# Optimization experiments

Measured on AMD Instinct MI355X. Metric: run time of the kernel, lower is better.

## Reference

```python
import jax, jax.numpy as jnp
import numpy as np

EPS = 1e-12  # torch F.normalize clamp_min eps


def _linear_interp(t, M):
    # PyTorch F.interpolate(mode='linear', align_corners=False) along last axis.
    L = t.shape[-1]
    src = (jnp.arange(M, dtype=t.dtype) + 0.5) * (L / M) - 0.5
    src = jnp.maximum(src, 0.0)
    i0 = jnp.minimum(jnp.floor(src).astype(jnp.int32), L - 1)
    i1 = jnp.minimum(i0 + 1, L - 1)
    frac = src - i0.astype(t.dtype)
    return t[..., i0] * (1.0 - frac) + t[..., i1] * frac


def _l2norm(t):
    n = jnp.linalg.norm(t, axis=-1, keepdims=True)
    return t / jnp.maximum(n, EPS)


def setup_inputs() -> dict:
    key = jax.random.key(0)
    ks = jax.random.split(key, 6)
    b, dim, m = 4, 512, 4096
    h = w = 64
    heads = 8
    s = 0.02
    return {
        "x": jax.random.normal(ks[0], (b, dim, m), dtype=jnp.float32),
        "y": jax.random.normal(ks[1], (b, dim, h, w), dtype=jnp.float32),
        "temperature": jnp.ones((heads, 1, 1), dtype=jnp.float32),
        "w_kv": jax.random.normal(ks[2], (2 * dim, dim), dtype=jnp.float32) * s,
        "w_q": jax.random.normal(ks[3], (dim, dim), dtype=jnp.float32) * s,
        "w_dw": jax.random.normal(ks[4], (dim, dim, 3, 3), dtype=jnp.float32) * s,
        "w_out": jax.random.normal(ks[5], (dim, dim), dtype=jnp.float32) * s,
    }


def reference(x, y, temperature, w_kv, w_q, w_dw, w_out):
    b, c, m = x.shape
    heads = temperature.shape[0]
    hd = c // heads

    # kv = Conv1d(dim, 2*dim, k=1)(x); split into k, v
    kv = jnp.einsum('bcm,oc->bom', x, w_kv)
    k, v = jnp.split(kv, 2, axis=1)

    # q = dwconv3x3(Conv2d 1x1(y)) -> flatten -> linear-resize to m
    q = jnp.einsum('bchw,oc->bohw', y, w_q)
    q = jax.lax.conv_general_dilated(
        q, w_dw, window_strides=(1, 1), padding=[(1, 1), (1, 1)],
        dimension_numbers=('NCHW', 'OIHW', 'NCHW'))
    q = q.reshape(b, c, -1)
    q = _linear_interp(q, m)

    # split heads: [b, head, c', m]
    q = _l2norm(q.reshape(b, heads, hd, m))
    k = _l2norm(k.reshape(b, heads, hd, m))
    v = v.reshape(b, heads, hd, m)

    # channel-wise attention: [b, head, c', c']
    attn = jnp.einsum('bhcm,bhdm->bhcd', q, k) * temperature
    attn = jax.nn.softmax(attn, axis=-1)
    out = jnp.einsum('bhcd,bhdm->bhcm', attn, v).reshape(b, c, m)

    # project_out: Conv1d k=1
    return jnp.einsum('bcm,oc->bom', out, w_out)
```

## Files before the change

### kernel.cpp

```cpp
#include <hip/hip_runtime.h>
#include <hip/hip_bf16.h>
#include <math.h>

typedef float f32x4 __attribute__((ext_vector_type(4)));
typedef int   i32x4 __attribute__((ext_vector_type(4)));
typedef short s16x8 __attribute__((ext_vector_type(8)));

#define NB 4
#define NC 512
#define NM 4096
#define NHEADS 8

#define GLDS16(src, dst) __builtin_amdgcn_global_load_lds( \
    (const __attribute__((address_space(1))) void*)(src),  \
    (__attribute__((address_space(3))) void*)(dst), 16, 0, 0)

__device__ __forceinline__ float b2f(unsigned short u) {
  union { unsigned int i; float f; } x; x.i = ((unsigned)u) << 16; return x.f;
}

__global__ __launch_bounds__(256) void transpose_k(
    const float* __restrict__ x, const float* __restrict__ y,
    __hip_bfloat16* __restrict__ xT, __hip_bfloat16* __restrict__ yT)
{
  __shared__ __hip_bfloat16 tile[64][65];
  int z = blockIdx.z;
  const float* src = ((z < 4) ? x : y) + (long)(z & 3) * ((long)NC * NM);
  __hip_bfloat16* dst = (z < 4 ? xT : yT) + (long)(z & 3) * ((long)NC * NM);
  int tm = blockIdx.x * 64, tc = blockIdx.y * 64;
  int tx = threadIdx.x & 63, ty = threadIdx.x >> 6;
  #pragma unroll
  for (int p = 0; p < 16; p++) {
    int row = ty + p * 4;
    tile[row][tx] = __float2bfloat16(src[(long)(tc + row) * NM + tm + tx]);
  }
  __syncthreads();
  #pragma unroll
  for (int p = 0; p < 16; p++) {
    int row = ty + p * 4;
    dst[(long)(tm + row) * NC + tc + tx] = tile[tx][row];
  }
}

__global__ __launch_bounds__(256) void pack_wdw(
    const float* __restrict__ wdw, __hip_bfloat16* __restrict__ Wr)
{
  long idx = (long)blockIdx.x * 256 + threadIdx.x;
  if (idx < 9L * 512 * 512) {
    int r = (int)(idx >> 18);
    int rem = (int)(idx & 262143);
    int o = rem >> 9, i = rem & 511;
    Wr[idx] = __float2bfloat16(wdw[((long)o * 512 + i) * 9 + r]);
  }
}

__global__ __launch_bounds__(256) void convert_w(
    const float* __restrict__ wkv, const float* __restrict__ wq,
    __hip_bfloat16* __restrict__ wkvB, __hip_bfloat16* __restrict__ wqT)
{
  long idx = (long)blockIdx.x * 256 + threadIdx.x;
  if (idx < 524288) {
    wkvB[idx] = __float2bfloat16(wkv[idx]);
  } else if (idx < 524288 + 262144) {
    long j = idx - 524288;
    int c = (int)(j >> 9), cp = (int)(j & 511);
    wqT[j] = __float2bfloat16(wq[(long)cp * 512 + c]);
  }
}

__global__ __launch_bounds__(256) void gemm_bt(
    const __hip_bfloat16* __restrict__ Aall, long sA,
    const __hip_bfloat16* __restrict__ Ball, long sB,
    __hip_bfloat16* __restrict__ Cball, float* __restrict__ Cfall, long sC,
    int M, int N, int Kd, int outF32)
{
  const __hip_bfloat16* A = Aall + (long)blockIdx.z * sA;
  const __hip_bfloat16* B = Ball + (long)blockIdx.z * sB;
  const int m0 = blockIdx.y * 128, n0 = blockIdx.x * 128;
  __shared__ __hip_bfloat16 As[128 * 32];
  __shared__ __hip_bfloat16 Bs[128 * 32];
  const int tid = threadIdx.x;
  const int wid = tid >> 6, lane = tid & 63;
  const int wm = (wid >> 1) * 64, wn = (wid & 1) * 64;
  const int quad = lane >> 4, l16 = lane & 15;
  const int srow = wid * 32 + (lane >> 2);
  const int scol = (lane & 3) * 8;
  f32x4 acc[4][4] = {};
  for (int k0 = 0; k0 < Kd; k0 += 32) {
    __syncthreads();
    #pragma unroll
    for (int t = 0; t < 2; t++) {
      GLDS16(A + (long)(m0 + srow + t * 16) * Kd + k0 + scol,
             As + (wid * 32 + t * 16) * 32);
      GLDS16(B + (long)(n0 + srow + t * 16) * Kd + k0 + scol,
             Bs + (wid * 32 + t * 16) * 32);
    }
    __builtin_amdgcn_s_waitcnt(0);
    __syncthreads();
    s16x8 bfr[4];
    #pragma unroll
    for (int j = 0; j < 4; j++)
      bfr[j] = *(const s16x8*)(&Bs[(wn + j * 16 + l16) * 32 + quad * 8]);
    #pragma unroll
    for (int i = 0; i < 4; i++) {
      s16x8 af = *(const s16x8*)(&As[(wm + i * 16 + l16) * 32 + quad * 8]);
      #pragma unroll
      for (int j = 0; j < 4; j++)
        acc[i][j] = __builtin_amdgcn_mfma_f32_16x16x32_bf16(af, bfr[j], acc[i][j], 0, 0, 0);
    }
  }
  if (outF32) {
    float* C = Cfall + (long)blockIdx.z * sC;
    #pragma unroll
    for (int i = 0; i < 4; i++)
      #pragma unroll
      for (int j = 0; j < 4; j++) {
        int rbase = m0 + wm + i * 16 + quad * 4;
        int col = n0 + wn + j * 16 + l16;
        #pragma unroll
        for (int r = 0; r < 4; r++)
          C[(long)(rbase + r) * N + col] = acc[i][j][r];
      }
  } else {
    __hip_bfloat16* C = Cball + (long)blockIdx.z * sC;
    #pragma unroll
    for (int i = 0; i < 4; i++)
      #pragma unroll
      for (int j = 0; j < 4; j++) {
        int rbase = m0 + wm + i * 16 + quad * 4;
        int col = n0 + wn + j * 16 + l16;
        #pragma unroll
        for (int r = 0; r < 4; r++)
          C[(long)(rbase + r) * N + col] = __float2bfloat16(acc[i][j][r]);
      }
  }
}

__global__ __launch_bounds__(256) void conv3x3(
    const __hip_bfloat16* __restrict__ Wt,
    const __hip_bfloat16* __restrict__ yT,
    const __hip_bfloat16* __restrict__ zeropad,
    __hip_bfloat16* __restrict__ q2)
{
  const int b = blockIdx.z;
  const int n0 = blockIdx.x * 128;
  const int m0 = blockIdx.y * 128;
  __shared__ __hip_bfloat16 As3[3 * 128 * 32];
  __shared__ __hip_bfloat16 Bs[256 * 32];
  const int tid = threadIdx.x;
  const int wid = tid >> 6, lane = tid & 63;
  const int wm = (wid >> 1) * 64, wn = (wid & 1) * 64;
  const int quad = lane >> 4, l16 = lane & 15;
  const int lrow = lane >> 2, scol = (lane & 3) * 8;
  const int h0 = n0 >> 6;
  const __hip_bfloat16* yb = yT + (long)b * NM * NC;
  f32x4 acc[4][4] = {};
  const s16x8 zero8 = {0, 0, 0, 0, 0, 0, 0, 0};

  for (int ic = 0; ic < 512; ic += 32) {
    #pragma unroll
    for (int g = 0; g < 3; g++) {
      __syncthreads();
      if (g == 0) {
        #pragma unroll
        for (int t = 0; t < 4; t++) {
          int p = wid * 64 + t * 16 + lrow;
          int hw = (h0 - 1) * 64 + p;
          const __hip_bfloat16* src = (((unsigned)hw) < (unsigned)NM)
              ? (yb + (long)hw * NC + ic + scol) : (zeropad + scol % 8);
          GLDS16(src, Bs + (wid * 64 + t * 16) * 32);
        }
      }
      #pragma unroll
      for (int t = 0; t < 3; t++) {
        int r = g * 3 + t;
        #pragma unroll
        for (int t2 = 0; t2 < 2; t2++) {
          GLDS16(Wt + ((long)r * 512 + m0 + wid * 32 + t2 * 16 + lrow) * 512 + ic + scol,
                 As3 + (t * 128 + wid * 32 + t2 * 16) * 32);
        }
      }
      __builtin_amdgcn_s_waitcnt(0);
      __syncthreads();
      const int dy = g - 1;
      #pragma unroll
      for (int t = 0; t < 3; t++) {
        const int dx = t - 1;
        s16x8 bfr[4];
        #pragma unroll
        for (int j = 0; j < 4; j++) {
          int nl = wn + j * 16 + l16;
          int wq_ = nl & 63, hr = nl >> 6;
          int wp = wq_ + dx;
          bool v = ((unsigned)wp) < 64u;
          int p = v ? ((hr + 1 + dy) * 64 + wp) : 0;
          s16x8 tt = *(const s16x8*)(&Bs[p * 32 + quad * 8]);
          bfr[j] = v ? tt : zero8;
        }
        #pragma unroll
        for (int i = 0; i < 4; i++) {
          s16x8 af = *(const s16x8*)(&As3[(t * 128 + wm + i * 16 + l16) * 32 + quad * 8]);
          #pragma unroll
          for (int j = 0; j < 4; j++)
            acc[i][j] = __builtin_amdgcn_mfma_f32_16x16x32_bf16(af, bfr[j], acc[i][j], 0, 0, 0);
        }
      }
    }
  }
  __hip_bfloat16* Cb = q2 + (long)b * NC * NM;
  #pragma unroll
  for (int i = 0; i < 4; i++) {
    #pragma unroll
    for (int j = 0; j < 4; j++) {
      int rbase = m0 + wm + i * 16 + quad * 4;
      int col = n0 + wn + j * 16 + l16;
      #pragma unroll
      for (int r = 0; r < 4; r++)
        Cb[(long)(rbase + r) * NM + col] = __float2bfloat16(acc[i][j][r]);
    }
  }
}

__global__ __launch_bounds__(256) void rowsumsq(
    const __hip_bfloat16* __restrict__ X, float* __restrict__ out)
{
  long row = blockIdx.x;
  const __hip_bfloat16* p = X + row * (long)NM + threadIdx.x * 16;
  union { i32x4 v; unsigned short u[8]; } a, b;
  a.v = *(const i32x4*)(p);
  b.v = *(const i32x4*)(p + 8);
  float s = 0.f;
  #pragma unroll
  for (int t = 0; t < 8; t++) {
    float f0 = b2f(a.u[t]); s += f0 * f0;
    float f1 = b2f(b.u[t]); s += f1 * f1;
  }
  #pragma unroll
  for (int off = 32; off > 0; off >>= 1) s += __shfl_down(s, off);
  __shared__ float red[4];
  if ((threadIdx.x & 63) == 0) red[threadIdx.x >> 6] = s;
  __syncthreads();
  if (threadIdx.x == 0)
    out[row] = fmaxf(sqrtf(red[0] + red[1] + red[2] + red[3]), 1e-12f);
}

__global__ __launch_bounds__(256) void attn_g(
    const __hip_bfloat16* __restrict__ q2, const __hip_bfloat16* __restrict__ Kb,
    float* __restrict__ Gpart)
{
  const int mc = blockIdx.x, h = blockIdx.y, b = blockIdx.z;
  const __hip_bfloat16* qrow = q2 + ((long)b * NC + h * 64) * NM + mc * 512;
  const __hip_bfloat16* krow = Kb + ((long)b * NC + h * 64) * NM + mc * 512;
  __shared__ __hip_bfloat16 Qs[64 * 40];
  __shared__ __hip_bfloat16 Ks[64 * 40];
  const int tid = threadIdx.x;
  const int wid = tid >> 6, lane = tid & 63;
  const int wc = (wid >> 1) * 32, wd = (wid & 1) * 32;
  const int quad = lane >> 4, l16 = lane & 15;
  const int srow = tid >> 2, scol = (tid & 3) * 8;
  f32x4 acc[2][2] = {};
  for (int k0 = 0; k0 < 512; k0 += 32) {
    __syncthreads();
    *(i32x4*)(&Qs[srow * 40 + scol]) = *(const i32x4*)(&qrow[(long)srow * NM + k0 + scol]);
    *(i32x4*)(&Ks[srow * 40 + scol]) = *(const i32x4*)(&krow[(long)srow * NM + k0 + scol]);
    __syncthreads();
    s16x8 bfr[2];
    #pragma unroll
    for (int j = 0; j < 2; j++)
      bfr[j] = *(const s16x8*)(&Ks[(wd + j * 16 + l16) * 40 + quad * 8]);
    #pragma unroll
    for (int i = 0; i < 2; i++) {
      s16x8 af = *(const s16x8*)(&Qs[(wc + i * 16 + l16) * 40 + quad * 8]);
      #pragma unroll
      for (int j = 0; j < 2; j++)
        acc[i][j] = __builtin_amdgcn_mfma_f32_16x16x32_bf16(af, bfr[j], acc[i][j], 0, 0, 0);
    }
  }
  float* gp = Gpart + ((long)((b * 8 + h) * 8 + mc)) * 4096;
  #pragma unroll
  for (int i = 0; i < 2; i++)
    #pragma unroll
    for (int j = 0; j < 2; j++)
      #pragma unroll
      for (int r = 0; r < 4; r++)
        gp[(wc + i * 16 + quad * 4 + r) * 64 + wd + j * 16 + l16] = acc[i][j][r];
}

__global__ __launch_bounds__(256) void softmax_attn(
    const float* __restrict__ Gpart, const float* __restrict__ qn,
    const float* __restrict__ kn, const float* __restrict__ temp,
    float* __restrict__ attn)
{
  const int h = blockIdx.x, b = blockIdx.y;
  __shared__ float G[64][64];
  const int tid = threadIdx.x;
  const float tv = temp[h];
  for (int e = tid; e < 4096; e += 256) {
    float s = 0.f;
    #pragma unroll
    for (int p = 0; p < 8; p++)
      s += Gpart[((long)((b * 8 + h) * 8 + p)) * 4096 + e];
    int c = e >> 6, d = e & 63;
    float scale = tv / (qn[b * 512 + h * 64 + c] * kn[b * 512 + h * 64 + d]);
    G[c][d] = s * scale;
  }
  __syncthreads();
  int row = tid >> 2, s4 = tid & 3;
  float mx = -1e30f;
  for (int d = s4; d < 64; d += 4) mx = fmaxf(mx, G[row][d]);
  mx = fmaxf(mx, __shfl_xor(mx, 1));
  mx = fmaxf(mx, __shfl_xor(mx, 2));
  float sum = 0.f;
  for (int d = s4; d < 64; d += 4) { float e = __expf(G[row][d] - mx); G[row][d] = e; sum += e; }
  sum += __shfl_xor(sum, 1);
  sum += __shfl_xor(sum, 2);
  float inv = 1.f / sum;
  float* ap = attn + ((long)(b * 8 + h)) * 4096;
  for (int d = s4; d < 64; d += 4) ap[row * 64 + d] = G[row][d] * inv;
}

__global__ __launch_bounds__(256) void wa_kernel(
    const float* __restrict__ attn, const float* __restrict__ wout,
    __hip_bfloat16* __restrict__ Wa)
{
  const int oc = blockIdx.x, h = blockIdx.y, b = blockIdx.z;
  __shared__ float At[64][64];
  __shared__ float Wtl[64][65];
  const int tid = threadIdx.x;
  const float* ap = attn + ((long)(b * 8 + h)) * 4096;
  for (int e = tid; e < 4096; e += 256) {
    At[e >> 6][e & 63] = ap[e];
    Wtl[e >> 6][e & 63] = wout[(long)(oc * 64 + (e >> 6)) * 512 + h * 64 + (e & 63)];
  }
  __syncthreads();
  int d = tid & 63, og = tid >> 6;
  #pragma unroll
  for (int k = 0; k < 16; k++) {
    int o = og * 16 + k;
    float s = 0.f;
    #pragma unroll 8
    for (int c = 0; c < 64; c++) s += Wtl[o][c] * At[c][d];
    Wa[((long)b * 512 + oc * 64 + o) * 512 + h * 64 + d] = __float2bfloat16(s);
  }
}

extern "C" void kernel_launch(void* const* d_in, const int* in_sizes, int n_in,
                              void* d_out, int out_size, void* d_ws, size_t ws_size,
                              hipStream_t stream) {
  const float* x    = (const float*)d_in[0];
  const float* y    = (const float*)d_in[1];
  const float* temp = (const float*)d_in[2];
  const float* wkv  = (const float*)d_in[3];
  const float* wq   = (const float*)d_in[4];
  const float* wdw  = (const float*)d_in[5];
  const float* wout = (const float*)d_in[6];
  float* out = (float*)d_out;

  char* ws = (char*)d_ws;
  const long TEN = 16777216;
  __hip_bfloat16* xT  = (__hip_bfloat16*)(ws);
  __hip_bfloat16* q2  = xT;
  __hip_bfloat16* yT  = (__hip_bfloat16*)(ws + TEN);
  float* Gpart        = (float*)(ws + TEN);
  float* attn         = (float*)(ws + TEN + 4194304);
  __hip_bfloat16* Wa  = (__hip_bfloat16*)(ws + TEN + 4718592);
  float* knorm        = (float*)(ws + TEN + 6815744);
  float* qnorm        = (float*)(ws + TEN + 6823936);
  __hip_bfloat16* Kb  = (__hip_bfloat16*)(ws + 2 * TEN);
  __hip_bfloat16* Vt  = (__hip_bfloat16*)(ws + 3 * TEN);
  __hip_bfloat16* Wfold = (__hip_bfloat16*)(ws + 4 * TEN);
  __hip_bfloat16* Wr    = (__hip_bfloat16*)(ws + 4 * TEN + 4718592);
  __hip_bfloat16* wkvB  = (__hip_bfloat16*)(ws + 4 * TEN + 9437184);
  __hip_bfloat16* wqT   = (__hip_bfloat16*)(ws + 4 * TEN + 10485760);
  __hip_bfloat16* zeropad = (__hip_bfloat16*)(ws + 4 * TEN + 11010048);

  const long S = (long)4096 * 512;
  const long S2 = (long)512 * 512;
  dim3 blk(256);

  hipMemsetAsync(zeropad, 0, 256, stream);
  pack_wdw<<<dim3(9216), blk, 0, stream>>>(wdw, Wr);
  convert_w<<<dim3(3072), blk, 0, stream>>>(wkv, wq, wkvB, wqT);
  transpose_k<<<dim3(64, 8, 8), blk, 0, stream>>>(x, y, xT, yT);
  gemm_bt<<<dim3(4, 4, 9), blk, 0, stream>>>(Wr, S2, wqT, 0L, Wfold, nullptr, S2, 512, 512, 512, 0);
  gemm_bt<<<dim3(32, 4, 4), blk, 0, stream>>>(wkvB, 0L, xT, S, Kb, nullptr, S, 512, 4096, 512, 0);
  gemm_bt<<<dim3(4, 32, 4), blk, 0, stream>>>(xT, S, wkvB + 512 * 512, 0L, Vt, nullptr, S, 4096, 512, 512, 0);
  conv3x3<<<dim3(32, 4, 4), blk, 0, stream>>>(Wfold, yT, zeropad, q2);
  rowsumsq<<<dim3(2048), blk, 0, stream>>>(Kb, knorm);
  rowsumsq<<<dim3(2048), blk, 0, stream>>>(q2, qnorm);
  attn_g<<<dim3(8, 8, 4), blk, 0, stream>>>(q2, Kb, Gpart);
  softmax_attn<<<dim3(8, 4), blk, 0, stream>>>(Gpart, qnorm, knorm, temp, attn);
  wa_kernel<<<dim3(8, 8, 4), blk, 0, stream>>>(attn, wout, Wa);
  gemm_bt<<<dim3(32, 4, 4), blk, 0, stream>>>(Wa, S2, Vt, S, nullptr, out, S, 512, 4096, 512, 1);
  (void)in_sizes; (void)n_in; (void)out_size; (void)ws_size;
}
```

Measured before the change: 321.5 us.

## Fuse norms into GEMM epilogues, merge prep kernels, K/V GEMM, and softmax with Wa

Row sum-of-squares for K and Q are now accumulated with atomics in the GEMM and conv epilogues, which removes two separate rowsumsq passes over bf16 tensors. The weight-conversion kernels and the memset are merged into one prep kernel that also zeroes the norm buffers. K and V projections run in one gemm_kv launch, and softmax is fused with the Wa computation. The transpose is vectorized with float4 loads and ushort4 stores. In exchange, the norms now come from fp32 accumulators rather than rounded bf16 values, the atomics make summation order nondeterministic, and the softmax is recomputed redundantly in each of the eight oc blocks.

```diff
diff --git a/kernel.cpp b/kernel.cpp
--- a/kernel.cpp
+++ b/kernel.cpp
@@ -15,56 +15,59 @@
     (const __attribute__((address_space(1))) void*)(src),  \
     (__attribute__((address_space(3))) void*)(dst), 16, 0, 0)
 
-__device__ __forceinline__ float b2f(unsigned short u) {
-  union { unsigned int i; float f; } x; x.i = ((unsigned)u) << 16; return x.f;
+__global__ __launch_bounds__(256) void prep(
+    const float* __restrict__ wdw, const float* __restrict__ wkv,
+    const float* __restrict__ wq,
+    __hip_bfloat16* __restrict__ Wr, __hip_bfloat16* __restrict__ wkvB,
+    __hip_bfloat16* __restrict__ wqT, __hip_bfloat16* __restrict__ zeropad,
+    float* __restrict__ norms)
+{
+  long idx = (long)blockIdx.x * 256 + threadIdx.x;
+  if (idx < 2359296) {
+    int r = (int)(idx / 262144);
+    int rem = (int)(idx % 262144);
+    int o = rem >> 9, i = rem & 511;
+    Wr[idx] = __float2bfloat16(wdw[((long)o * 512 + i) * 9 + r]);
+  } else if (idx < 2883584) {
+    long j = idx - 2359296;
+    wkvB[j] = __float2bfloat16(wkv[j]);
+  } else if (idx < 3145728) {
+    long j = idx - 2883584;
+    int c = (int)(j >> 9), cp = (int)(j & 511);
+    wqT[j] = __float2bfloat16(wq[(long)cp * 512 + c]);
+  } else if (idx < 3145856) {
+    zeropad[idx - 3145728] = __float2bfloat16(0.f);
+  } else if (idx < 3149952) {
+    norms[idx - 3145856] = 0.f;
+  }
 }
 
 __global__ __launch_bounds__(256) void transpose_k(
     const float* __restrict__ x, const float* __restrict__ y,
     __hip_bfloat16* __restrict__ xT, __hip_bfloat16* __restrict__ yT)
 {
-  __shared__ __hip_bfloat16 tile[64][65];
+  __shared__ __hip_bfloat16 tile[64][68];
   int z = blockIdx.z;
   const float* src = ((z < 4) ? x : y) + (long)(z & 3) * ((long)NC * NM);
   __hip_bfloat16* dst = (z < 4 ? xT : yT) + (long)(z & 3) * ((long)NC * NM);
   int tm = blockIdx.x * 64, tc = blockIdx.y * 64;
-  int tx = threadIdx.x & 63, ty = threadIdx.x >> 6;
-  #pragma unroll
-  for (int p = 0; p < 16; p++) {
-    int row = ty + p * 4;
-    tile[row][tx] = __float2bfloat16(src[(long)(tc + row) * NM + tm + tx]);
+  int tx4 = threadIdx.x & 15, trow = threadIdx.x >> 4;
+  #pragma unroll
+  for (int p = 0; p < 4; p++) {
+    int crow = trow + p * 16;
+    f32x4 v = *(const f32x4*)&src[(long)(tc + crow) * NM + tm + tx4 * 4];
+    #pragma unroll
+    for (int t = 0; t < 4; t++) tile[crow][tx4 * 4 + t] = __float2bfloat16(v[t]);
   }
   __syncthreads();
   #pragma unroll
-  for (int p = 0; p < 16; p++) {
-    int row = ty + p * 4;
-    dst[(long)(tm + row) * NC + tc + tx] = tile[tx][row];
-  }
-}
-
-__global__ __launch_bounds__(256) void pack_wdw(
-    const float* __restrict__ wdw, __hip_bfloat16* __restrict__ Wr)
-{
-  long idx = (long)blockIdx.x * 256 + threadIdx.x;
-  if (idx < 9L * 512 * 512) {
-    int r = (int)(idx >> 18);
-    int rem = (int)(idx & 262143);
-    int o = rem >> 9, i = rem & 511;
-    Wr[idx] = __float2bfloat16(wdw[((long)o * 512 + i) * 9 + r]);
-  }
-}
-
-__global__ __launch_bounds__(256) void convert_w(
-    const float* __restrict__ wkv, const float* __restrict__ wq,
-    __hip_bfloat16* __restrict__ wkvB, __hip_bfloat16* __restrict__ wqT)
-{
-  long idx = (long)blockIdx.x * 256 + threadIdx.x;
-  if (idx < 524288) {
-    wkvB[idx] = __float2bfloat16(wkv[idx]);
-  } else if (idx < 524288 + 262144) {
-    long j = idx - 524288;
-    int c = (int)(j >> 9), cp = (int)(j & 511);
-    wqT[j] = __float2bfloat16(wq[(long)cp * 512 + c]);
+  for (int p = 0; p < 4; p++) {
+    int mrow = trow + p * 16;
+    union { ushort4 u4; unsigned short u[4]; } o;
+    #pragma unroll
+    for (int t = 0; t < 4; t++)
+      o.u[t] = *(const unsigned short*)&tile[tx4 * 4 + t][mrow];
+    *(ushort4*)&dst[(long)(tm + mrow) * NC + tc + tx4 * 4] = o.u4;
   }
 }
 
@@ -136,11 +139,88 @@
   }
 }
 
+__global__ __launch_bounds__(256) void gemm_kv(
+    const __hip_bfloat16* __restrict__ wkvB,
+    const __hip_bfloat16* __restrict__ xT,
+    __hip_bfloat16* __restrict__ Kb,
+    __hip_bfloat16* __restrict__ Vt,
+    float* __restrict__ knorm2)
+{
+  const int z = blockIdx.z;
+  const int b = z & 3;
+  const bool kmode = (z < 4);
+  const long S = (long)NM * NC;
+  const __hip_bfloat16* A = kmode ? wkvB : (xT + b * S);
+  const __hip_bfloat16* B = kmode ? (xT + b * S) : (wkvB + 262144);
+  __hip_bfloat16* C = kmode ? (Kb + b * S) : (Vt + b * S);
+  const int m0 = (kmode ? blockIdx.y : blockIdx.x) * 128;
+  const int n0 = (kmode ? blockIdx.x : blockIdx.y) * 128;
+  const int N = kmode ? NM : NC;
+  __shared__ __hip_bfloat16 As[128 * 32];
+  __shared__ __hip_bfloat16 Bs[128 * 32];
+  const int tid = threadIdx.x;
+  const int wid = tid >> 6, lane = tid & 63;
+  const int wm = (wid >> 1) * 64, wn = (wid & 1) * 64;
+  const int quad = lane >> 4, l16 = lane & 15;
+  const int srow = wid * 32 + (lane >> 2);
+  const int scol = (lane & 3) * 8;
+  f32x4 acc[4][4] = {};
+  for (int k0 = 0; k0 < NC; k0 += 32) {
+    __syncthreads();
+    #pragma unroll
+    for (int t = 0; t < 2; t++) {
+      GLDS16(A + (long)(m0 + srow + t * 16) * NC + k0 + scol,
+             As + (wid * 32 + t * 16) * 32);
+      GLDS16(B + (long)(n0 + srow + t * 16) * NC + k0 + scol,
+             Bs + (wid * 32 + t * 16) * 32);
+    }
+    __builtin_amdgcn_s_waitcnt(0);
+    __syncthreads();
+    s16x8 bfr[4];
+    #pragma unroll
+    for (int j = 0; j < 4; j++)
+      bfr[j] = *(const s16x8*)(&Bs[(wn + j * 16 + l16) * 32 + quad * 8]);
+    #pragma unroll
+    for (int i = 0; i < 4; i++) {
+      s16x8 af = *(const s16x8*)(&As[(wm + i * 16 + l16) * 32 + quad * 8]);
+      #pragma unroll
+      for (int j = 0; j < 4; j++)
+        acc[i][j] = __builtin_amdgcn_mfma_f32_16x16x32_bf16(af, bfr[j], acc[i][j], 0, 0, 0);
+    }
+  }
+  #pragma unroll
+  for (int i = 0; i < 4; i++)
+    #pragma unroll
+    for (int j = 0; j < 4; j++) {
+      int rbase = m0 + wm + i * 16 + quad * 4;
+      int col = n0 + wn + j * 16 + l16;
+      #pragma unroll
+      for (int r = 0; r < 4; r++)
+        C[(long)(rbase + r) * N + col] = __float2bfloat16(acc[i][j][r]);
+    }
+  if (kmode) {
+    #pragma unroll
+    for (int i = 0; i < 4; i++) {
+      int rbase = m0 + wm + i * 16 + quad * 4;
+      #pragma unroll
+      for (int r = 0; r < 4; r++) {
+        float s = 0.f;
+        #pragma unroll
+        for (int j = 0; j < 4; j++) s += acc[i][j][r] * acc[i][j][r];
+        s += __shfl_xor(s, 1); s += __shfl_xor(s, 2);
+        s += __shfl_xor(s, 4); s += __shfl_xor(s, 8);
+        if (l16 == 0) atomicAdd(&knorm2[b * 512 + rbase + r], s);
+      }
+    }
+  }
+}
+
 __global__ __launch_bounds__(256) void conv3x3(
     const __hip_bfloat16* __restrict__ Wt,
     const __hip_bfloat16* __restrict__ yT,
     const __hip_bfloat16* __restrict__ zeropad,
-    __hip_bfloat16* __restrict__ q2)
+    __hip_bfloat16* __restrict__ q2,
+    float* __restrict__ qnorm2)
 {
   const int b = blockIdx.z;
   const int n0 = blockIdx.x * 128;
@@ -209,7 +289,7 @@
   }
   __hip_bfloat16* Cb = q2 + (long)b * NC * NM;
   #pragma unroll
-  for (int i = 0; i < 4; i++) {
+  for (int i = 0; i < 4; i++)
     #pragma unroll
     for (int j = 0; j < 4; j++) {
       int rbase = m0 + wm + i * 16 + quad * 4;
@@ -218,30 +298,19 @@
       for (int r = 0; r < 4; r++)
         Cb[(long)(rbase + r) * NM + col] = __float2bfloat16(acc[i][j][r]);
     }
-  }
-}
-
-__global__ __launch_bounds__(256) void rowsumsq(
-    const __hip_bfloat16* __restrict__ X, float* __restrict__ out)
-{
-  long row = blockIdx.x;
-  const __hip_bfloat16* p = X + row * (long)NM + threadIdx.x * 16;
-  union { i32x4 v; unsigned short u[8]; } a, b;
-  a.v = *(const i32x4*)(p);
-  b.v = *(const i32x4*)(p + 8);
-  float s = 0.f;
-  #pragma unroll
-  for (int t = 0; t < 8; t++) {
-    float f0 = b2f(a.u[t]); s += f0 * f0;
-    float f1 = b2f(b.u[t]); s += f1 * f1;
-  }
-  #pragma unroll
-  for (int off = 32; off > 0; off >>= 1) s += __shfl_down(s, off);
-  __shared__ float red[4];
-  if ((threadIdx.x & 63) == 0) red[threadIdx.x >> 6] = s;
-  __syncthreads();
-  if (threadIdx.x == 0)
-    out[row] = fmaxf(sqrtf(red[0] + red[1] + red[2] + red[3]), 1e-12f);
+  #pragma unroll
+  for (int i = 0; i < 4; i++) {
+    int rbase = m0 + wm + i * 16 + quad * 4;
+    #pragma unroll
+    for (int r = 0; r < 4; r++) {
+      float s = 0.f;
+      #pragma unroll
+      for (int j = 0; j < 4; j++) s += acc[i][j][r] * acc[i][j][r];
+      s += __shfl_xor(s, 1); s += __shfl_xor(s, 2);
+      s += __shfl_xor(s, 4); s += __shfl_xor(s, 8);
+      if (l16 == 0) atomicAdd(&qnorm2[b * 512 + rbase + r], s);
+    }
+  }
 }
 
 __global__ __launch_bounds__(256) void attn_g(
@@ -286,13 +355,14 @@
         gp[(wc + i * 16 + quad * 4 + r) * 64 + wd + j * 16 + l16] = acc[i][j][r];
 }
 
-__global__ __launch_bounds__(256) void softmax_attn(
-    const float* __restrict__ Gpart, const float* __restrict__ qn,
-    const float* __restrict__ kn, const float* __restrict__ temp,
-    float* __restrict__ attn)
-{
-  const int h = blockIdx.x, b = blockIdx.y;
+__global__ __launch_bounds__(256) void softmax_wa(
+    const float* __restrict__ Gpart, const float* __restrict__ qnorm2,
+    const float* __restrict__ knorm2, const float* __restrict__ temp,
+    const float* __restrict__ wout, __hip_bfloat16* __restrict__ Wa)
+{
+  const int oc = blockIdx.x, h = blockIdx.y, b = blockIdx.z;
   __shared__ float G[64][64];
+  __shared__ float Wt[64][65];
   const int tid = threadIdx.x;
   const float tv = temp[h];
   for (int e = tid; e < 4096; e += 256) {
@@ -301,8 +371,10 @@
     for (int p = 0; p < 8; p++)
       s += Gpart[((long)((b * 8 + h) * 8 + p)) * 4096 + e];
     int c = e >> 6, d = e & 63;
-    float scale = tv / (qn[b * 512 + h * 64 + c] * kn[b * 512 + h * 64 + d]);
-    G[c][d] = s * scale;
+    float qn = fmaxf(sqrtf(qnorm2[b * 512 + h * 64 + c]), 1e-12f);
+    float kn = fmaxf(sqrtf(knorm2[b * 512 + h * 64 + d]), 1e-12f);
+    G[c][d] = s * tv / (qn * kn);
+    Wt[c][d] = wout[(long)(oc * 64 + c) * 512 + h * 64 + d];
   }
   __syncthreads();
   int row = tid >> 2, s4 = tid & 3;
@@ -315,31 +387,15 @@
   sum += __shfl_xor(sum, 1);
   sum += __shfl_xor(sum, 2);
   float inv = 1.f / sum;
-  float* ap = attn + ((long)(b * 8 + h)) * 4096;
-  for (int d = s4; d < 64; d += 4) ap[row * 64 + d] = G[row][d] * inv;
-}
-
-__global__ __launch_bounds__(256) void wa_kernel(
-    const float* __restrict__ attn, const float* __restrict__ wout,
-    __hip_bfloat16* __restrict__ Wa)
-{
-  const int oc = blockIdx.x, h = blockIdx.y, b = blockIdx.z;
-  __shared__ float At[64][64];
-  __shared__ float Wtl[64][65];
-  const int tid = threadIdx.x;
-  const float* ap = attn + ((long)(b * 8 + h)) * 4096;
-  for (int e = tid; e < 4096; e += 256) {
-    At[e >> 6][e & 63] = ap[e];
-    Wtl[e >> 6][e & 63] = wout[(long)(oc * 64 + (e >> 6)) * 512 + h * 64 + (e & 63)];
-  }
+  for (int d = s4; d < 64; d += 4) G[row][d] *= inv;
   __syncthreads();
   int d = tid & 63, og = tid >> 6;
   #pragma unroll
-  for (int k = 0; k < 16; k++) {
-    int o = og * 16 + k;
+  for (int k2 = 0; k2 < 16; k2++) {
+    int o = og * 16 + k2;
     float s = 0.f;
     #pragma unroll 8
-    for (int c = 0; c < 64; c++) s += Wtl[o][c] * At[c][d];
+    for (int c = 0; c < 64; c++) s += Wt[o][c] * G[c][d];
     Wa[((long)b * 512 + oc * 64 + o) * 512 + h * 64 + d] = __float2bfloat16(s);
   }
 }
@@ -362,10 +418,7 @@
   __hip_bfloat16* q2  = xT;
   __hip_bfloat16* yT  = (__hip_bfloat16*)(ws + TEN);
   float* Gpart        = (float*)(ws + TEN);
-  float* attn         = (float*)(ws + TEN + 4194304);
   __hip_bfloat16* Wa  = (__hip_bfloat16*)(ws + TEN + 4718592);
-  float* knorm        = (float*)(ws + TEN + 6815744);
-  float* qnorm        = (float*)(ws + TEN + 6823936);
   __hip_bfloat16* Kb  = (__hip_bfloat16*)(ws + 2 * TEN);
   __hip_bfloat16* Vt  = (__hip_bfloat16*)(ws + 3 * TEN);
   __hip_bfloat16* Wfold = (__hip_bfloat16*)(ws + 4 * TEN);
@@ -373,24 +426,21 @@
   __hip_bfloat16* wkvB  = (__hip_bfloat16*)(ws + 4 * TEN + 9437184);
   __hip_bfloat16* wqT   = (__hip_bfloat16*)(ws + 4 * TEN + 10485760);
   __hip_bfloat16* zeropad = (__hip_bfloat16*)(ws + 4 * TEN + 11010048);
+  float* norms          = (float*)(ws + 4 * TEN + 11010304);
+  float* knorm2 = norms;
+  float* qnorm2 = norms + 2048;
 
   const long S = (long)4096 * 512;
   const long S2 = (long)512 * 512;
   dim3 blk(256);
 
-  hipMemsetAsync(zeropad, 0, 256, stream);
-  pack_wdw<<<dim3(9216), blk, 0, stream>>>(wdw, Wr);
-  convert_w<<<dim3(3072), blk, 0, stream>>>(wkv, wq, wkvB, wqT);
+  prep<<<dim3(12305), blk, 0, stream>>>(wdw, wkv, wq, Wr, wkvB, wqT, zeropad, norms);
   transpose_k<<<dim3(64, 8, 8), blk, 0, stream>>>(x, y, xT, yT);
   gemm_bt<<<dim3(4, 4, 9), blk, 0, stream>>>(Wr, S2, wqT, 0L, Wfold, nullptr, S2, 512, 512, 512, 0);
-  gemm_bt<<<dim3(32, 4, 4), blk, 0, stream>>>(wkvB, 0L, xT, S, Kb, nullptr, S, 512, 4096, 512, 0);
-  gemm_bt<<<dim3(4, 32, 4), blk, 0, stream>>>(xT, S, wkvB + 512 * 512, 0L, Vt, nullptr, S, 4096, 512, 512, 0);
-  conv3x3<<<dim3(32, 4, 4), blk, 0, stream>>>(Wfold, yT, zeropad, q2);
-  rowsumsq<<<dim3(2048), blk, 0, stream>>>(Kb, knorm);
-  rowsumsq<<<dim3(2048), blk, 0, stream>>>(q2, qnorm);
+  gemm_kv<<<dim3(32, 4, 8), blk, 0, stream>>>(wkvB, xT, Kb, Vt, knorm2);
+  conv3x3<<<dim3(32, 4, 4), blk, 0, stream>>>(Wfold, yT, zeropad, q2, qnorm2);
   attn_g<<<dim3(8, 8, 4), blk, 0, stream>>>(q2, Kb, Gpart);
-  softmax_attn<<<dim3(8, 4), blk, 0, stream>>>(Gpart, qnorm, knorm, temp, attn);
-  wa_kernel<<<dim3(8, 8, 4), blk, 0, stream>>>(attn, wout, Wa);
+  softmax_wa<<<dim3(8, 8, 4), blk, 0, stream>>>(Gpart, qnorm2, knorm2, temp, wout, Wa);
   gemm_bt<<<dim3(32, 4, 4), blk, 0, stream>>>(Wa, S2, Vt, S, nullptr, out, S, 512, 4096, 512, 1);
   (void)in_sizes; (void)n_in; (void)out_size; (void)ws_size;
 }
```

Result: faster. 311.1 us (-3.2%).
